# Kernel tuning notes

Measured on AMD Instinct MI355X. Metric: run time of the kernel, lower is better.

The kernel has to match this reference:

```python
import jax, jax.numpy as jnp
import numpy as np

N_HEAD = 8
HEAD_HIDDEN = 16
NODE_HIDDEN = 128
EDGE_HIDDEN = 64


def setup_inputs() -> dict:
    key = jax.random.key(0)
    ks = jax.random.split(key, 12)
    b, n = 2, 512
    hd = N_HEAD * HEAD_HIDDEN
    s = 0.05
    x = jax.random.normal(ks[0], (b, n, NODE_HIDDEN), dtype=jnp.float32)
    edge_attr = jax.random.normal(ks[1], (b, n, n, EDGE_HIDDEN), dtype=jnp.float32)
    mask = jax.random.randint(ks[2], (b, n), 0, 2) > 0
    Wqkv = jax.random.normal(ks[3], (NODE_HIDDEN, 3 * hd), dtype=jnp.float32) * s
    bqkv = jax.random.normal(ks[4], (3 * hd,), dtype=jnp.float32) * s
    We = jax.random.normal(ks[5], (EDGE_HIDDEN, hd), dtype=jnp.float32) * s
    be = jax.random.normal(ks[6], (hd,), dtype=jnp.float32) * s
    Wno = jax.random.normal(ks[7], (hd, NODE_HIDDEN), dtype=jnp.float32) * s
    bno = jax.random.normal(ks[8], (NODE_HIDDEN,), dtype=jnp.float32) * s
    Weo = jax.random.normal(ks[9], (hd, EDGE_HIDDEN), dtype=jnp.float32) * s
    beo = jax.random.normal(ks[10], (EDGE_HIDDEN,), dtype=jnp.float32) * s
    return {"x": x, "edge_attr": edge_attr, "mask": mask,
            "Wqkv": Wqkv, "bqkv": bqkv, "We": We, "be": be,
            "Wno": Wno, "bno": bno, "Weo": Weo, "beo": beo}


def reference(x, edge_attr, mask, Wqkv, bqkv, We, be, Wno, bno, Weo, beo):
    b, n, _ = x.shape
    h, d = N_HEAD, HEAD_HIDDEN
    qkv = x @ Wqkv + bqkv                      # b n 3hd
    q, k, v = jnp.split(qkv, 3, axis=-1)
    e = edge_attr @ We + be                    # b i j (h d)
    q = q.reshape(b, n, 1, h, d)               # b i 1 h d
    k = k.reshape(b, 1, n, h, d)               # b 1 j h d
    v = v.reshape(b, n, h, d)                  # b j h d
    e = e.reshape(b, n, n, h, d)               # b i j h d
    raw_att = q * k * e                        # b i j h d (reused for edge_out)
    att = raw_att.sum(axis=-1) / np.float32(np.sqrt(d))  # b i j h
    neg = -jnp.finfo(att.dtype).max
    att = jnp.where(mask[:, None, :, None], att, neg)
    att = jax.nn.softmax(att, axis=-2)         # softmax over j
    node = jnp.einsum('bijh,bjhd->bihd', att, v).reshape(b, n, h * d)
    node_out = node @ Wno + bno
    edge_out = raw_att.reshape(b, n, n, h * d) @ Weo + beo
    return node_out, edge_out
```

## Files before the change

### kernel.cpp

```cpp
#include <hip/hip_runtime.h>
#include <hip/hip_bf16.h>
#include <stdint.h>

#define NN 512
#define HD 128

typedef __attribute__((ext_vector_type(8))) short bf16x8;
typedef __attribute__((ext_vector_type(4))) float f32x4;

static __device__ __forceinline__ float bf2f(unsigned short u) {
  union { uint32_t u32; float f; } cv; cv.u32 = ((uint32_t)u) << 16; return cv.f;
}
static __device__ __forceinline__ unsigned short f2bf(float f) {
  union { float f; uint32_t u; } cv; cv.f = f;
  return (unsigned short)((cv.u + 0x7FFFu + ((cv.u >> 16) & 1u)) >> 16);
}
static __device__ __forceinline__ uint32_t cvtpk(float lo, float hi) {
  uint32_t r;
  asm("v_cvt_pk_bf16_f32 %0, %1, %2" : "=v"(r) : "v"(lo), "v"(hi));
  return r;
}

struct DetectArgs { const uint16_t* p[10]; int n[10]; };

__global__ __launch_bounds__(256) void detect_kernel(DetectArgs a, int* __restrict__ flags) {
  __shared__ int acc[256];
  const int ti = blockIdx.x;
  int n = a.n[ti]; if (n > 2048) n = 2048;
  int g = 0;
  for (int w = threadIdx.x; w < n; w += 256) {
    uint16_t v = a.p[ti][w];
    int e = (v >> 7) & 0xFF;
    g += (v == 0u || (e >= 90 && e <= 133)) ? 1 : 0;
  }
  acc[threadIdx.x] = g;
  __syncthreads();
  for (int s = 128; s > 0; s >>= 1) {
    if (threadIdx.x < s) acc[threadIdx.x] += acc[threadIdx.x + s];
    __syncthreads();
  }
  if (threadIdx.x == 0) flags[ti] = (acc[0] * 10 < n * 9) ? 1 : 0;
}

__global__ __launch_bounds__(256) void prep_kernel(const uint32_t* __restrict__ raw,
                                                   float* __restrict__ mbias, int count,
                                                   const void* __restrict__ Weop,
                                                   const int* __restrict__ flags,
                                                   uint16_t* __restrict__ w2f) {
  if (blockIdx.x < 4) {
    int inspect = count >> 2; if (inspect > 256) inspect = 256;
    bool ok_i32 = true, ok_f32 = true, ok_bf16 = true;
    #pragma unroll 1
    for (int w = 0; w < inspect; ++w) {
      uint32_t v = raw[w];
      if (v > 1u) ok_i32 = false;
      if (!(v == 0u || v == 0x3F800000u)) ok_f32 = false;
      uint32_t lo = v & 0xFFFFu, hi = v >> 16;
      if (!((lo == 0u || lo == 0x3F80u) && (hi == 0u || hi == 0x3F80u))) ok_bf16 = false;
    }
    int idx = blockIdx.x * 256 + threadIdx.x;
    if (idx < count) {
      bool on;
      if (ok_i32 || ok_f32) on = raw[idx] != 0u;
      else if (ok_bf16)     on = ((const uint16_t*)raw)[idx] != 0u;
      else                  on = ((const uint8_t*)raw)[idx] != 0u;
      mbias[idx] = on ? 0.0f : -1e30f;
    }
  } else {
    const int slot = (blockIdx.x - 4) * 256 + threadIdx.x;
    const int t2 = slot >> 8, s = (slot >> 6) & 3, ln = slot & 63;
    const int c = t2 * 16 + (ln & 15);
    const int k0 = s * 32 + ((ln >> 4) & 3) * 8;
    const int f_Weo = flags[8];
    bf16x8 fr;
    if (f_Weo) {
      const float* W = (const float*)Weop;
      #pragma unroll
      for (int e = 0; e < 8; ++e) fr[e] = (short)f2bf(W[(k0 + e) * 64 + c]);
    } else {
      const uint16_t* W = (const uint16_t*)Weop;
      #pragma unroll
      for (int e = 0; e < 8; ++e) fr[e] = (short)W[(k0 + e) * 64 + c];
    }
    *(bf16x8*)&w2f[slot * 8] = fr;
  }
}

__global__ __launch_bounds__(128) void qkv_kernel(const void* __restrict__ xp,
                                                  const void* __restrict__ Wp,
                                                  const void* __restrict__ bp,
                                                  const int* __restrict__ flags,
                                                  uint16_t* __restrict__ qf,
                                                  uint16_t* __restrict__ kf,
                                                  uint16_t* __restrict__ vf) {
  const int f_x = flags[0], f_W = flags[2], f_b = flags[3];
  const int row = blockIdx.x;
  const int t = threadIdx.x;
  __shared__ float xs[HD];
  xs[t] = f_x ? ((const float*)xp)[row * HD + t] : bf2f(((const uint16_t*)xp)[row * HD + t]);
  __syncthreads();
  float aq = 0.f, ak = 0.f, av = 0.f;
  if (f_W) {
    const float* W = (const float*)Wp;
    #pragma unroll 4
    for (int kk = 0; kk < HD; ++kk) {
      float xv = xs[kk]; const float* wr = W + kk * 384;
      aq = fmaf(xv, wr[t], aq);
      ak = fmaf(xv, wr[128 + t], ak);
      av = fmaf(xv, wr[256 + t], av);
    }
  } else {
    const uint16_t* W = (const uint16_t*)Wp;
    #pragma unroll 4
    for (int kk = 0; kk < HD; ++kk) {
      float xv = xs[kk]; const uint16_t* wr = W + kk * 384;
      aq = fmaf(xv, bf2f(wr[t]), aq);
      ak = fmaf(xv, bf2f(wr[128 + t]), ak);
      av = fmaf(xv, bf2f(wr[256 + t]), av);
    }
  }
  float bq = f_b ? ((const float*)bp)[t]       : bf2f(((const uint16_t*)bp)[t]);
  float bk = f_b ? ((const float*)bp)[128 + t] : bf2f(((const uint16_t*)bp)[128 + t]);
  float bv = f_b ? ((const float*)bp)[256 + t] : bf2f(((const uint16_t*)bp)[256 + t]);
  qf[row * HD + t] = f2bf(aq + bq);
  kf[row * HD + ((t & 15) << 3) + (t >> 4)] = f2bf(ak + bk);
  vf[((size_t)((row >> 9) * HD + t)) * NN + (row & (NN - 1))] = f2bf(av + bv);
}

__global__ __launch_bounds__(512, 4) void gat_main_kernel(
    const void* __restrict__ eap,
    const void* __restrict__ Wep,  const void* __restrict__ bep,
    const void* __restrict__ Wnop, const void* __restrict__ bnop,
    const void* __restrict__ beop,
    const int* __restrict__ flags,
    const uint16_t* __restrict__ qf, const uint16_t* __restrict__ kf,
    const uint16_t* __restrict__ vf, const uint16_t* __restrict__ w2f,
    const float* __restrict__ mbias,
    float* __restrict__ node_out, float* __restrict__ edge_out) {
  const int tid = threadIdx.x;
  const int w = tid >> 6, lane = tid & 63;
  const int l15 = lane & 15, quad = lane >> 4;
  const int bb = blockIdx.x >> 9;
  const int i  = blockIdx.x & (NN - 1);
  const int f_ea = flags[1], f_We = flags[4], f_be = flags[5];
  const int f_Wno = flags[6], f_bno = flags[7], f_beo = flags[9];

  __shared__ __align__(16) uint16_t B1f[8 * 2 * 64 * 8];
  __shared__ __align__(16) uint16_t BLf[4 * 64 * 8];
  __shared__ __align__(16) uint16_t pool[8 * 1152];
  __shared__ __align__(16) uint16_t att_s[8 * 520];
  __shared__ __align__(16) float q_s[HD];
  __shared__ __align__(16) float beq_s[HD];
  __shared__ __align__(16) float beo_s[64];
  __shared__ __align__(16) float node_s[HD];

  if (tid < HD) q_s[tid] = bf2f(qf[(bb * NN + i) * HD + tid]);
  if (tid >= 128 && tid < 192) {
    int c = tid - 128;
    beo_s[c] = f_beo ? ((const float*)beop)[c] : bf2f(((const uint16_t*)beop)[c]);
  }
  if (tid < 256) {
    const int s = tid >> 6, ln = tid & 63;
    const int head = s * 2 + ((ln >> 5) & 1);
    const short v = ((ln & 15) == head) ? (short)0x3F80 : (short)0;
    bf16x8 fr;
    #pragma unroll
    for (int e = 0; e < 8; ++e) fr[e] = v;
    *(bf16x8*)&BLf[(s * 64 + ln) * 8] = fr;
  }
  __syncthreads();

  if (tid < HD) {
    float b = f_be ? ((const float*)bep)[tid] : bf2f(((const uint16_t*)bep)[tid]);
    beq_s[tid] = b * q_s[tid];
  }
  for (int slot = tid; slot < 1024; slot += 512) {
    const int t = slot >> 7, s = (slot >> 6) & 1, ln = slot & 63;
    const int c = t * 16 + (ln & 15);
    const int k0 = s * 32 + (ln >> 4) * 8;
    const float qc = q_s[c];
    bf16x8 fr;
    if (f_We) {
      const float* W = (const float*)Wep;
      #pragma unroll
      for (int e = 0; e < 8; ++e) fr[e] = (short)f2bf(W[(k0 + e) * HD + c] * qc);
    } else {
      const uint16_t* W = (const uint16_t*)Wep;
      #pragma unroll
      for (int e = 0; e < 8; ++e) fr[e] = (short)f2bf(bf2f(W[(k0 + e) * HD + c]) * qc);
    }
    *(bf16x8*)&B1f[slot * 8] = fr;
  }
  __syncthreads();

  const size_t io_base = (size_t)(bb * NN + i) * NN * 64;
  const uint16_t* kperm = kf + (size_t)bb * NN * HD;
  const float* mrow = mbias + bb * NN;
  uint16_t* rws = pool + w * 1152;
  float*    fws = (float*)rws;

  for (int band = w; band < 32; band += 8) {
    const int j0 = band * 16;
    const f32x4 mr = *(const f32x4*)(mrow + j0 + quad * 4);
    bf16x8 k8[4];
    #pragma unroll
    for (int r = 0; r < 4; ++r)
      k8[r] = *(const bf16x8*)(kperm + (size_t)(j0 + quad * 4 + r) * HD + l15 * 8);

    bf16x8 A1[2];
    if (f_ea) {
      const float* ea = (const float*)eap + io_base + (size_t)(j0 + l15) * 64 + quad * 8;
      f32x4 e0 = __builtin_nontemporal_load((const f32x4*)ea);
      f32x4 e1 = __builtin_nontemporal_load((const f32x4*)(ea + 4));
      f32x4 e2 = __builtin_nontemporal_load((const f32x4*)(ea + 32));
      f32x4 e3 = __builtin_nontemporal_load((const f32x4*)(ea + 36));
      union { bf16x8 v; uint32_t u[4]; } c0, c1;
      c0.u[0] = cvtpk(e0[0], e0[1]); c0.u[1] = cvtpk(e0[2], e0[3]);
      c0.u[2] = cvtpk(e1[0], e1[1]); c0.u[3] = cvtpk(e1[2], e1[3]);
      c1.u[0] = cvtpk(e2[0], e2[1]); c1.u[1] = cvtpk(e2[2], e2[3]);
      c1.u[2] = cvtpk(e3[0], e3[1]); c1.u[3] = cvtpk(e3[2], e3[3]);
      A1[0] = c0.v; A1[1] = c1.v;
    } else {
      const uint16_t* ea = (const uint16_t*)eap + io_base + (size_t)(j0 + l15) * 64 + quad * 8;
      A1[0] = __builtin_nontemporal_load((const bf16x8*)ea);
      A1[1] = __builtin_nontemporal_load((const bf16x8*)(ea + 32));
    }

    f32x4 acc2[4];
    #pragma unroll
    for (int t2 = 0; t2 < 4; ++t2) {
      const float bv = beo_s[t2 * 16 + l15];
      acc2[t2] = (f32x4){bv, bv, bv, bv};
    }
    f32x4 aL = {0.f, 0.f, 0.f, 0.f};

    #pragma unroll
    for (int h = 0; h < 2; ++h) {
      #pragma unroll
      for (int tl = 0; tl < 4; ++tl) {
        const int t = h * 4 + tl;
        const float bv = beq_s[t * 16 + l15];
        f32x4 a = {bv, bv, bv, bv};
        a = __builtin_amdgcn_mfma_f32_16x16x32_bf16(
              A1[0], *(const bf16x8*)&B1f[(t * 2 + 0) * 512 + lane * 8], a, 0, 0, 0);
        a = __builtin_amdgcn_mfma_f32_16x16x32_bf16(
              A1[1], *(const bf16x8*)&B1f[(t * 2 + 1) * 512 + lane * 8], a, 0, 0, 0);
        const float v0 = a[0] * bf2f((unsigned short)k8[0][t]);
        const float v1 = a[1] * bf2f((unsigned short)k8[1][t]);
        const float v2 = a[2] * bf2f((unsigned short)k8[2][t]);
        const float v3 = a[3] * bf2f((unsigned short)k8[3][t]);
        const uint32_t p01 = cvtpk(v0, v1), p23 = cvtpk(v2, v3);
        uint16_t* rp = &rws[(tl ^ quad) * 16 + l15];
        rp[(quad * 4 + 0) * 72] = (uint16_t)p01;
        rp[(quad * 4 + 1) * 72] = (uint16_t)(p01 >> 16);
        rp[(quad * 4 + 2) * 72] = (uint16_t)p23;
        rp[(quad * 4 + 3) * 72] = (uint16_t)(p23 >> 16);
      }
      #pragma unroll
      for (int sl = 0; sl < 2; ++sl) {
        const int s = h * 2 + sl;
        const int blk = (sl * 2 + (quad >> 1)) ^ (l15 >> 2);
        const bf16x8 A2 = *(const bf16x8*)&rws[l15 * 72 + blk * 16 + (quad & 1) * 8];
        aL = __builtin_amdgcn_mfma_f32_16x16x32_bf16(
               A2, *(const bf16x8*)&BLf[(s * 64 + lane) * 8], aL, 0, 0, 0);
        #pragma unroll
        for (int t2 = 0; t2 < 4; ++t2)
          acc2[t2] = __builtin_amdgcn_mfma_f32_16x16x32_bf16(
                       A2, *(const bf16x8*)&w2f[(size_t)((t2 * 4 + s) * 64 + lane) * 8],
                       acc2[t2], 0, 0, 0);
      }
    }

    if (l15 < 8) {
      #pragma unroll
      for (int r = 0; r < 4; ++r)
        att_s[l15 * 520 + (j0 + quad * 4 + r)] = f2bf(aL[r] * 0.25f + mr[r]);
    }

    #pragma unroll
    for (int ch = 0; ch < 2; ++ch) {
      #pragma unroll
      for (int t2l = 0; t2l < 2; ++t2l) {
        const int t2 = ch * 2 + t2l;
        #pragma unroll
        for (int r = 0; r < 4; ++r)
          fws[(quad * 4 + r) * 36 + t2l * 16 + l15] = acc2[t2][r];
      }
      #pragma unroll
      for (int rg = 0; rg < 2; ++rg) {
        const int row = rg * 8 + (lane >> 3);
        f32x4 vv = *(const f32x4*)&fws[row * 36 + (lane & 7) * 4];
        __builtin_nontemporal_store(vv,
            (f32x4*)(edge_out + io_base + (size_t)(j0 + row) * 64 + ch * 32) + (lane & 7));
      }
    }
  }
  __syncthreads();

  {
    float vals[8];
    float m = -3.4e38f;
    #pragma unroll
    for (int it = 0; it < 8; ++it)
      m = fmaxf(m, bf2f(att_s[w * 520 + it * 64 + lane]));
    #pragma unroll
    for (int off = 32; off; off >>= 1) m = fmaxf(m, __shfl_xor(m, off));
    float ssum = 0.f;
    #pragma unroll
    for (int it = 0; it < 8; ++it) {
      float v = __expf(bf2f(att_s[w * 520 + it * 64 + lane]) - m);
      vals[it] = v; ssum += v;
    }
    #pragma unroll
    for (int off = 32; off; off >>= 1) ssum += __shfl_xor(ssum, off);
    const float inv = 1.0f / ssum;
    #pragma unroll
    for (int it = 0; it < 8; ++it)
      att_s[w * 520 + it * 64 + lane] = f2bf(vals[it] * inv);
  }
  __syncthreads();

  {
    f32x4 nacc[8];
    #pragma unroll
    for (int t = 0; t < 8; ++t) nacc[t] = (f32x4){0.f, 0.f, 0.f, 0.f};
    const uint16_t* vbase = vf + (size_t)bb * HD * NN;
    #pragma unroll
    for (int ks = 0; ks < 2; ++ks) {
      const int k0 = w * 64 + ks * 32;
      const bf16x8 Af = *(const bf16x8*)&att_s[(l15 & 7) * 520 + k0 + quad * 8];
      #pragma unroll
      for (int t = 0; t < 8; ++t) {
        const bf16x8 Bf = *(const bf16x8*)(vbase + (size_t)(t * 16 + l15) * NN + k0 + quad * 8);
        nacc[t] = __builtin_amdgcn_mfma_f32_16x16x32_bf16(Af, Bf, nacc[t], 0, 0, 0);
      }
    }
    float* red = (float*)pool;
    #pragma unroll
    for (int t = 0; t < 8; ++t)
      if (quad == (t >> 2)) red[w * 128 + t * 16 + l15] = nacc[t][t & 3];
    __syncthreads();
    if (tid < HD) {
      float s = 0.f;
      #pragma unroll
      for (int w2 = 0; w2 < 8; ++w2) s += red[w2 * 128 + tid];
      node_s[tid] = s;
    }
    __syncthreads();
  }

  {
    const int c = tid & 127, part = tid >> 7;
    float acc = 0.f;
    if (f_Wno) {
      const float* W = (const float*)Wnop;
      #pragma unroll 8
      for (int kk = part * 32; kk < part * 32 + 32; ++kk)
        acc = fmaf(node_s[kk], W[kk * HD + c], acc);
    } else {
      const uint16_t* W = (const uint16_t*)Wnop;
      #pragma unroll 8
      for (int kk = part * 32; kk < part * 32 + 32; ++kk)
        acc = fmaf(node_s[kk], bf2f(W[kk * HD + c]), acc);
    }
    float* red2 = (float*)pool + 1024;
    red2[tid] = acc;
    __syncthreads();
    if (tid < HD) {
      float b = f_bno ? ((const float*)bnop)[tid] : bf2f(((const uint16_t*)bnop)[tid]);
      float r = red2[tid] + red2[128 + tid] + red2[256 + tid] + red2[384 + tid] + b;
      node_out[(bb * NN + i) * HD + tid] = r;
    }
  }
}

extern "C" void kernel_launch(void* const* d_in, const int* in_sizes, int n_in,
                              void* d_out, int out_size, void* d_ws, size_t ws_size,
                              hipStream_t stream) {
  const int b = in_sizes[0] / (NN * HD);
  const int rows = b * NN;

  int*   flags = (int*)d_ws;
  float* mbias = (float*)((char*)d_ws + 64);
  uint16_t* qf = (uint16_t*)((char*)d_ws + 64 + 4096);
  uint16_t* kf = qf + (size_t)rows * HD;
  uint16_t* vf = kf + (size_t)rows * HD;
  uint16_t* w2f = vf + (size_t)rows * HD;

  float* node_out = (float*)d_out;
  float* edge_out = node_out + (size_t)rows * HD;

  DetectArgs da;
  const int float_idx[10] = {0, 1, 3, 4, 5, 6, 7, 8, 9, 10};
  for (int t = 0; t < 10; ++t) {
    da.p[t] = (const uint16_t*)d_in[float_idx[t]];
    da.n[t] = in_sizes[float_idx[t]];
  }

  detect_kernel<<<10, 256, 0, stream>>>(da, flags);
  prep_kernel<<<8, 256, 0, stream>>>((const uint32_t*)d_in[2], mbias, rows,
                                     d_in[9], flags, w2f);
  qkv_kernel<<<rows, 128, 0, stream>>>(d_in[0], d_in[3], d_in[4], flags, qf, kf, vf);
  gat_main_kernel<<<rows, 512, 0, stream>>>(d_in[1], d_in[5], d_in[6], d_in[7], d_in[8],
                                            d_in[10], flags,
                                            qf, kf, vf, w2f, mbias, node_out, edge_out);
}
```

Baseline: 360.2 us.

## Precompute We fragments globally and apply q scaling after MFMA instead of per-block

The per-row q-scaled We fragment build (B1f) is moved out of the main kernel. A prep kernel now writes an unscaled bf16 We fragment buffer once, and q is multiplied in fp32 after the MFMA together with k. The ones-matrix BLf shared buffer is replaced by register-built fragments, and q is stored permuted like k so each thread can read it with 32-bit loads. This removes a shared-memory setup phase, a sync and LDS footprint per block. In exchange, B operands are now read from global/L2 memory in the inner loop and k loads are split per half.

Measured after the change: 447.4 us. +24.2%, slower.

```diff
diff --git a/kernel.cpp b/kernel.cpp
--- a/kernel.cpp
+++ b/kernel.cpp
@@ -19,6 +19,9 @@
   uint32_t r;
   asm("v_cvt_pk_bf16_f32 %0, %1, %2" : "=v"(r) : "v"(lo), "v"(hi));
   return r;
+}
+static __device__ __forceinline__ float bfel(uint32_t u, int hi) {
+  return bf2f((unsigned short)(hi ? (u >> 16) : (u & 0xFFFFu)));
 }
 
 struct DetectArgs { const uint16_t* p[10]; int n[10]; };
@@ -45,8 +48,10 @@
 __global__ __launch_bounds__(256) void prep_kernel(const uint32_t* __restrict__ raw,
                                                    float* __restrict__ mbias, int count,
                                                    const void* __restrict__ Weop,
+                                                   const void* __restrict__ Wep,
                                                    const int* __restrict__ flags,
-                                                   uint16_t* __restrict__ w2f) {
+                                                   uint16_t* __restrict__ w2f,
+                                                   uint16_t* __restrict__ w1f) {
   if (blockIdx.x < 4) {
     int inspect = count >> 2; if (inspect > 256) inspect = 256;
     bool ok_i32 = true, ok_f32 = true, ok_bf16 = true;
@@ -66,7 +71,7 @@
       else                  on = ((const uint8_t*)raw)[idx] != 0u;
       mbias[idx] = on ? 0.0f : -1e30f;
     }
-  } else {
+  } else if (blockIdx.x < 8) {
     const int slot = (blockIdx.x - 4) * 256 + threadIdx.x;
     const int t2 = slot >> 8, s = (slot >> 6) & 3, ln = slot & 63;
     const int c = t2 * 16 + (ln & 15);
@@ -83,6 +88,23 @@
       for (int e = 0; e < 8; ++e) fr[e] = (short)W[(k0 + e) * 64 + c];
     }
     *(bf16x8*)&w2f[slot * 8] = fr;
+  } else {
+    const int slot = (blockIdx.x - 8) * 256 + threadIdx.x;
+    const int t = slot >> 7, s = (slot >> 6) & 1, ln = slot & 63;
+    const int c = t * 16 + (ln & 15);
+    const int k0 = s * 32 + (ln >> 4) * 8;
+    const int f_We = flags[4];
+    bf16x8 fr;
+    if (f_We) {
+      const float* W = (const float*)Wep;
+      #pragma unroll
+      for (int e = 0; e < 8; ++e) fr[e] = (short)f2bf(W[(k0 + e) * HD + c]);
+    } else {
+      const uint16_t* W = (const uint16_t*)Wep;
+      #pragma unroll
+      for (int e = 0; e < 8; ++e) fr[e] = (short)W[(k0 + e) * HD + c];
+    }
+    *(bf16x8*)&w1f[slot * 8] = fr;
   }
 }
 
@@ -122,19 +144,20 @@
   float bq = f_b ? ((const float*)bp)[t]       : bf2f(((const uint16_t*)bp)[t]);
   float bk = f_b ? ((const float*)bp)[128 + t] : bf2f(((const uint16_t*)bp)[128 + t]);
   float bv = f_b ? ((const float*)bp)[256 + t] : bf2f(((const uint16_t*)bp)[256 + t]);
-  qf[row * HD + t] = f2bf(aq + bq);
+  qf[row * HD + ((t & 15) << 3) + (t >> 4)] = f2bf(aq + bq);
   kf[row * HD + ((t & 15) << 3) + (t >> 4)] = f2bf(ak + bk);
   vf[((size_t)((row >> 9) * HD + t)) * NN + (row & (NN - 1))] = f2bf(av + bv);
 }
 
 __global__ __launch_bounds__(512, 4) void gat_main_kernel(
     const void* __restrict__ eap,
-    const void* __restrict__ Wep,  const void* __restrict__ bep,
+    const void* __restrict__ bep,
     const void* __restrict__ Wnop, const void* __restrict__ bnop,
     const void* __restrict__ beop,
     const int* __restrict__ flags,
     const uint16_t* __restrict__ qf, const uint16_t* __restrict__ kf,
-    const uint16_t* __restrict__ vf, const uint16_t* __restrict__ w2f,
+    const uint16_t* __restrict__ vf, const uint16_t* __restrict__ w1f,
+    const uint16_t* __restrict__ w2f,
     const float* __restrict__ mbias,
     float* __restrict__ node_out, float* __restrict__ edge_out) {
   const int tid = threadIdx.x;
@@ -142,59 +165,26 @@
   const int l15 = lane & 15, quad = lane >> 4;
   const int bb = blockIdx.x >> 9;
   const int i  = blockIdx.x & (NN - 1);
-  const int f_ea = flags[1], f_We = flags[4], f_be = flags[5];
+  const int f_ea = flags[1], f_be = flags[5];
   const int f_Wno = flags[6], f_bno = flags[7], f_beo = flags[9];
 
-  __shared__ __align__(16) uint16_t B1f[8 * 2 * 64 * 8];
-  __shared__ __align__(16) uint16_t BLf[4 * 64 * 8];
   __shared__ __align__(16) uint16_t pool[8 * 1152];
   __shared__ __align__(16) uint16_t att_s[8 * 520];
-  __shared__ __align__(16) float q_s[HD];
-  __shared__ __align__(16) float beq_s[HD];
+  __shared__ __align__(16) float be_s[HD];
   __shared__ __align__(16) float beo_s[64];
   __shared__ __align__(16) float node_s[HD];
 
-  if (tid < HD) q_s[tid] = bf2f(qf[(bb * NN + i) * HD + tid]);
+  if (tid < HD)
+    be_s[tid] = f_be ? ((const float*)bep)[tid] : bf2f(((const uint16_t*)bep)[tid]);
   if (tid >= 128 && tid < 192) {
     int c = tid - 128;
     beo_s[c] = f_beo ? ((const float*)beop)[c] : bf2f(((const uint16_t*)beop)[c]);
   }
-  if (tid < 256) {
-    const int s = tid >> 6, ln = tid & 63;
-    const int head = s * 2 + ((ln >> 5) & 1);
-    const short v = ((ln & 15) == head) ? (short)0x3F80 : (short)0;
-    bf16x8 fr;
-    #pragma unroll
-    for (int e = 0; e < 8; ++e) fr[e] = v;
-    *(bf16x8*)&BLf[(s * 64 + ln) * 8] = fr;
-  }
-  __syncthreads();
-
-  if (tid < HD) {
-    float b = f_be ? ((const float*)bep)[tid] : bf2f(((const uint16_t*)bep)[tid]);
-    beq_s[tid] = b * q_s[tid];
-  }
-  for (int slot = tid; slot < 1024; slot += 512) {
-    const int t = slot >> 7, s = (slot >> 6) & 1, ln = slot & 63;
-    const int c = t * 16 + (ln & 15);
-    const int k0 = s * 32 + (ln >> 4) * 8;
-    const float qc = q_s[c];
-    bf16x8 fr;
-    if (f_We) {
-      const float* W = (const float*)Wep;
-      #pragma unroll
-      for (int e = 0; e < 8; ++e) fr[e] = (short)f2bf(W[(k0 + e) * HD + c] * qc);
-    } else {
-      const uint16_t* W = (const uint16_t*)Wep;
-      #pragma unroll
-      for (int e = 0; e < 8; ++e) fr[e] = (short)f2bf(bf2f(W[(k0 + e) * HD + c]) * qc);
-    }
-    *(bf16x8*)&B1f[slot * 8] = fr;
-  }
   __syncthreads();
 
   const size_t io_base = (size_t)(bb * NN + i) * NN * 64;
   const uint16_t* kperm = kf + (size_t)bb * NN * HD;
+  const uint16_t* qrow  = qf + (size_t)(bb * NN + i) * HD;
   const float* mrow = mbias + bb * NN;
   uint16_t* rws = pool + w * 1152;
   float*    fws = (float*)rws;
@@ -202,10 +192,6 @@
   for (int band = w; band < 32; band += 8) {
     const int j0 = band * 16;
     const f32x4 mr = *(const f32x4*)(mrow + j0 + quad * 4);
-    bf16x8 k8[4];
-    #pragma unroll
-    for (int r = 0; r < 4; ++r)
-      k8[r] = *(const bf16x8*)(kperm + (size_t)(j0 + quad * 4 + r) * HD + l15 * 8);
 
     bf16x8 A1[2];
     if (f_ea) {
@@ -236,19 +222,30 @@
 
     #pragma unroll
     for (int h = 0; h < 2; ++h) {
+      const uint32_t* qp = (const uint32_t*)(qrow + l15 * 8 + h * 4);
+      const uint32_t q0 = qp[0], q1 = qp[1];
+      uint32_t kx0[4], kx1[4];
+      #pragma unroll
+      for (int r = 0; r < 4; ++r) {
+        const uint32_t* kp =
+            (const uint32_t*)(kperm + (size_t)(j0 + quad * 4 + r) * HD + l15 * 8 + h * 4);
+        kx0[r] = kp[0]; kx1[r] = kp[1];
+      }
+
       #pragma unroll
       for (int tl = 0; tl < 4; ++tl) {
         const int t = h * 4 + tl;
-        const float bv = beq_s[t * 16 + l15];
+        const float bv = be_s[t * 16 + l15];
         f32x4 a = {bv, bv, bv, bv};
         a = __builtin_amdgcn_mfma_f32_16x16x32_bf16(
-              A1[0], *(const bf16x8*)&B1f[(t * 2 + 0) * 512 + lane * 8], a, 0, 0, 0);
+              A1[0], *(const bf16x8*)&w1f[(size_t)((t * 2 + 0) * 64 + lane) * 8], a, 0, 0, 0);
         a = __builtin_amdgcn_mfma_f32_16x16x32_bf16(
-              A1[1], *(const bf16x8*)&B1f[(t * 2 + 1) * 512 + lane * 8], a, 0, 0, 0);
-        const float v0 = a[0] * bf2f((unsigned short)k8[0][t]);
-        const float v1 = a[1] * bf2f((unsigned short)k8[1][t]);
-        const float v2 = a[2] * bf2f((unsigned short)k8[2][t]);
-        const float v3 = a[3] * bf2f((unsigned short)k8[3][t]);
+              A1[1], *(const bf16x8*)&w1f[(size_t)((t * 2 + 1) * 64 + lane) * 8], a, 0, 0, 0);
+        const float qt = bfel((tl < 2) ? q0 : q1, tl & 1);
+        const float v0 = a[0] * qt * bfel((tl < 2) ? kx0[0] : kx1[0], tl & 1);
+        const float v1 = a[1] * qt * bfel((tl < 2) ? kx0[1] : kx1[1], tl & 1);
+        const float v2 = a[2] * qt * bfel((tl < 2) ? kx0[2] : kx1[2], tl & 1);
+        const float v3 = a[3] * qt * bfel((tl < 2) ? kx0[3] : kx1[3], tl & 1);
         const uint32_t p01 = cvtpk(v0, v1), p23 = cvtpk(v2, v3);
         uint16_t* rp = &rws[(tl ^ quad) * 16 + l15];
         rp[(quad * 4 + 0) * 72] = (uint16_t)p01;
@@ -261,8 +258,11 @@
         const int s = h * 2 + sl;
         const int blk = (sl * 2 + (quad >> 1)) ^ (l15 >> 2);
         const bf16x8 A2 = *(const bf16x8*)&rws[l15 * 72 + blk * 16 + (quad & 1) * 8];
-        aL = __builtin_amdgcn_mfma_f32_16x16x32_bf16(
-               A2, *(const bf16x8*)&BLf[(s * 64 + lane) * 8], aL, 0, 0, 0);
+        const short lv = (l15 == s * 2 + (quad >> 1)) ? (short)0x3F80 : (short)0;
+        bf16x8 Lf;
+        #pragma unroll
+        for (int e = 0; e < 8; ++e) Lf[e] = lv;
+        aL = __builtin_amdgcn_mfma_f32_16x16x32_bf16(A2, Lf, aL, 0, 0, 0);
         #pragma unroll
         for (int t2 = 0; t2 < 4; ++t2)
           acc2[t2] = __builtin_amdgcn_mfma_f32_16x16x32_bf16(
@@ -386,6 +386,7 @@
   uint16_t* kf = qf + (size_t)rows * HD;
   uint16_t* vf = kf + (size_t)rows * HD;
   uint16_t* w2f = vf + (size_t)rows * HD;
+  uint16_t* w1f = w2f + 1024 * 8;
 
   float* node_out = (float*)d_out;
   float* edge_out = node_out + (size_t)rows * HD;
@@ -398,10 +399,11 @@
   }
 
   detect_kernel<<<10, 256, 0, stream>>>(da, flags);
-  prep_kernel<<<8, 256, 0, stream>>>((const uint32_t*)d_in[2], mbias, rows,
-                                     d_in[9], flags, w2f);
+  prep_kernel<<<12, 256, 0, stream>>>((const uint32_t*)d_in[2], mbias, rows,
+                                      d_in[9], d_in[5], flags, w2f, w1f);
   qkv_kernel<<<rows, 128, 0, stream>>>(d_in[0], d_in[3], d_in[4], flags, qf, kf, vf);
-  gat_main_kernel<<<rows, 512, 0, stream>>>(d_in[1], d_in[5], d_in[6], d_in[7], d_in[8],
+  gat_main_kernel<<<rows, 512, 0, stream>>>(d_in[1], d_in[6], d_in[7], d_in[8],
                                             d_in[10], flags,
-                                            qf, kf, vf, w2f, mbias, node_out, edge_out);
-}
+                                            qf, kf, vf, w1f, w2f, mbias,
+                                            node_out, edge_out);
+}
```
